# Kernel optimization log

Measured on AMD Instinct MI355X. Metric: run time of the kernel, lower is better.

Reference implementation:

```python
import jax, jax.numpy as jnp
import numpy as np

A = 4096          # agents
N_OBJ = 8192      # objects
IN_DIM = 16       # input_dim
EMBED = 128       # embedding_dim
MAX_OBJ = 16      # max set size
DEG = 8           # communicate in-degree (constant, target-major edges)
OBS_DEG = 8       # observe degree
POS_DIM = 2
ORIG = IN_DIM + POS_DIM   # 18, decoded element dim
THRES = 0.02              # duplicate filter distance threshold


def setup_inputs() -> dict:
    key = jax.random.key(0)
    ks = jax.random.split(key, 16)
    def lin(k, fi, fo):
        return (jax.random.normal(k, (fi, fo), jnp.float32) / np.float32(np.sqrt(fi)))
    obj_x = jax.random.normal(ks[0], (N_OBJ, IN_DIM), jnp.float32)
    obj_pos = jax.random.uniform(ks[1], (N_OBJ, POS_DIM), jnp.float32) * 10.0
    agent_pos = jax.random.uniform(ks[2], (A, POS_DIM), jnp.float32) * 10.0
    # (agent, observe, object) edges: row0 = agent, row1 = object (as in the torch HeteroData)
    obs_tgt = jnp.repeat(jnp.arange(A), OBS_DEG)
    obs_src = jax.random.randint(ks[3], (A * OBS_DEG,), 0, N_OBJ)
    obs_edge_index = jnp.stack([obs_tgt, obs_src])
    # (agent, communicate, agent) edges: row0 = source j, row1 = target i; target-major, constant degree
    tgt = jnp.repeat(jnp.arange(A), DEG)
    src = (tgt + 1 + jnp.tile(jnp.arange(DEG), A)) % A
    comm_edge_index = jnp.stack([src, tgt])
    return dict(
        obj_x=obj_x, obj_pos=obj_pos, agent_pos=agent_pos,
        enc_W1=lin(ks[4], ORIG, EMBED), enc_b1=jnp.zeros((EMBED,), jnp.float32),
        enc_W2=lin(ks[5], EMBED, EMBED), enc_b2=jnp.zeros((EMBED,), jnp.float32),
        mdec_Ws=lin(ks[6], EMBED, MAX_OBJ + 1), mdec_bs=jnp.zeros((MAX_OBJ + 1,), jnp.float32),
        mdec_Wx=lin(ks[7], EMBED, MAX_OBJ * ORIG), mdec_bx=jnp.zeros((MAX_OBJ * ORIG,), jnp.float32),
        menc_W1=lin(ks[8], ORIG, EMBED), menc_b1=jnp.zeros((EMBED,), jnp.float32),
        menc_W2=lin(ks[9], EMBED, EMBED), menc_b2=jnp.zeros((EMBED,), jnp.float32),
        dec_Ws=lin(ks[10], EMBED, MAX_OBJ + 1), dec_bs=jnp.zeros((MAX_OBJ + 1,), jnp.float32),
        dec_Wx=lin(ks[11], EMBED, MAX_OBJ * ORIG), dec_bx=jnp.zeros((MAX_OBJ * ORIG,), jnp.float32),
        obs_edge_index=obs_edge_index, comm_edge_index=comm_edge_index,
    )


def reference(obj_x, obj_pos, agent_pos,
              enc_W1, enc_b1, enc_W2, enc_b2,
              mdec_Ws, mdec_bs, mdec_Wx, mdec_bx,
              menc_W1, menc_b1, menc_W2, menc_b2,
              dec_Ws, dec_bs, dec_Wx, dec_bx,
              obs_edge_index, comm_edge_index):
    nA = agent_pos.shape[0]
    # ---- EncodeGNN: edge_index.flip -> source = object (row1), target = agent (row0)
    o = obs_edge_index[1]
    a = obs_edge_index[0]
    # message: [x_j, posx_j - posa_i] (position='rel')
    msg = jnp.concatenate([obj_x[o], obj_pos[o] - agent_pos[a]], axis=-1)      # [E_obs, ORIG]
    h = jax.nn.relu(msg @ enc_W1 + enc_b1)
    enc = jax.ops.segment_sum(h, a, num_segments=nA) @ enc_W2 + enc_b2         # [A, EMBED]
    # ---- MergeGNN message: decode source embedding per communicate edge
    j = comm_edge_index[0]
    i = comm_edge_index[1]
    zj = enc[j]                                                                 # [E, EMBED]
    npred = jnp.argmax(zj @ mdec_Ws + mdec_bs, axis=-1)                         # predicted set size per edge
    elems = (zj @ mdec_Wx + mdec_bx).reshape(-1, MAX_OBJ, ORIG)                 # [E, MAX_OBJ, ORIG]
    # update_rel_pos: decoded_pos += pos_j - pos_i
    relpos = (agent_pos[j] - agent_pos[i])[:, None, :]
    elems = jnp.concatenate([elems[..., :-POS_DIM], elems[..., -POS_DIM:] + relpos], axis=-1)
    valid = jnp.arange(MAX_OBJ)[None, :] < npred[:, None]                       # [E, MAX_OBJ]
    # ---- aggregate: edges are target-major with constant degree -> per-agent candidate pool
    deg = comm_edge_index.shape[1] // nA
    K = deg * MAX_OBJ
    cand = elems.reshape(nA, K, ORIG)
    v = valid.reshape(nA, K)
    # filter_duplicates (pos_only=True): pairwise distance on last POS_DIM dims
    pos = cand[..., -POS_DIM:]
    D = jnp.linalg.norm(pos[:, :, None, :] - pos[:, None, :, :], axis=-1)       # [A, K, K]
    tri = jnp.triu(jnp.ones((K, K), bool), k=1)
    dup = (D < THRES) & tri[None] & v[:, :, None] & v[:, None, :]
    keep = v & ~jnp.any(dup, axis=1)                                            # column is dup of an earlier row
    cnt = jnp.cumsum(keep.astype(jnp.int32), axis=1)
    keep = keep & (cnt <= MAX_OBJ - 1)                                          # cap at max_n - 1 kept elements
    # merge_encoder: masked set encode per agent
    hm = jax.nn.relu(cand @ menc_W1 + menc_b1) * keep[..., None]
    merged = hm.sum(axis=1) @ menc_W2 + menc_b2                                 # [A, EMBED]
    # ---- final decoder
    n2 = jnp.argmax(merged @ dec_Ws + dec_bs, axis=-1)
    decoded = (merged @ dec_Wx + dec_bx).reshape(nA, MAX_OBJ, ORIG)
    mask = jnp.arange(MAX_OBJ)[None, :] < n2[:, None]
    decoded = decoded * mask[..., None]                                         # padded+masked ragged set
    batch = jnp.broadcast_to(jnp.arange(nA)[:, None], (nA, MAX_OBJ))
    return decoded, batch, mask
```

## Files before the change

### kernel.cpp

```cpp
#include <hip/hip_runtime.h>

#define A_N   4096
#define EMBED 128
#define MAXO  16
#define DEG   8
#define OBSD  8
#define ORIG  18
#define KCAND 128
#define G     4
#define NBLK  (A_N / G)
#define NTHR  512
#define EL    (MAXO * ORIG)
#define NQ    (MAXO + 1)
#define THRES2 (0.02f * 0.02f)

__global__ __launch_bounds__(320) void prep_kernel(
    const float* __restrict__ enc_W2, const float* __restrict__ enc_b2,
    const float* __restrict__ mdec_Wx, const float* __restrict__ mdec_Ws,
    const float* __restrict__ mdec_bx, const float* __restrict__ mdec_bs,
    const float* __restrict__ menc_W2, const float* __restrict__ menc_b2,
    const float* __restrict__ dec_Wx, const float* __restrict__ dec_Ws,
    const float* __restrict__ dec_bx, const float* __restrict__ dec_bs,
    float* __restrict__ fWxA, float* __restrict__ fbxA,
    float* __restrict__ fWsA, float* __restrict__ fbsA,
    float* __restrict__ fWxB, float* __restrict__ fbxB,
    float* __restrict__ fWsB, float* __restrict__ fbsB)
{
    const int b = blockIdx.x, tid = threadIdx.x;
    const int side = b / 129, r = b % 129;
    const float* W2 = side ? menc_W2 : enc_W2;
    const float* b2 = side ? menc_b2 : enc_b2;
    const float* Wx = side ? dec_Wx : mdec_Wx;
    const float* Ws = side ? dec_Ws : mdec_Ws;
    const float* bx = side ? dec_bx : mdec_bx;
    const float* bs = side ? dec_bs : mdec_bs;
    float* oWx = side ? fWxB : fWxA;
    float* obx = side ? fbxB : fbxA;
    float* oWs = side ? fWsB : fWsA;
    float* obs_ = side ? fbsB : fbsA;

    __shared__ float rv[EMBED];
    if (tid < EMBED) rv[tid] = (r < EMBED) ? W2[r * EMBED + tid] : b2[tid];
    __syncthreads();

    if (tid < EL) {
        float acc = 0.f;
        for (int t = 0; t < EMBED; ++t) acc += rv[t] * Wx[t * EL + tid];
        if (r < EMBED) oWx[r * EL + tid] = acc;
        else           obx[tid] = acc + bx[tid];
    } else if (tid < EL + NQ) {
        const int q = tid - EL;
        float acc = 0.f;
        for (int t = 0; t < EMBED; ++t) acc += rv[t] * Ws[t * NQ + q];
        if (r < EMBED) oWs[r * NQ + q] = acc;
        else           obs_[q] = acc + bs[q];
    }
}

__global__ __launch_bounds__(NTHR, 8) void enc512_kernel(
    const float* __restrict__ obj_x, const float* __restrict__ obj_pos,
    const float* __restrict__ agent_pos,
    const float* __restrict__ enc_W1, const float* __restrict__ enc_b1,
    const float* __restrict__ fWxA, const float* __restrict__ fbxA,
    const float* __restrict__ fWsA, const float* __restrict__ fbsA,
    const int* __restrict__ obs_edge,
    float* __restrict__ elems_base, int* __restrict__ npred_out,
    float2* __restrict__ pxy_base)
{
    const int blk = blockIdx.x, tid = threadIdx.x;
    const int i0  = blk * G;
    const int col = tid & 127, q = tid >> 7;

    __shared__ int    on[G][OBSD];
    __shared__ float  msg[G * OBSD][20];
    __shared__ float4 SG[EMBED];
    __shared__ float  Lp[4][G * NQ];
    __shared__ float  lgts[G][NQ];
    __shared__ float4 Pp[2][EL];

    if (tid < G * OBSD) {
        const int g = tid >> 3, d = tid & 7;
        on[g][d] = obs_edge[A_N * OBSD + (i0 + g) * OBSD + d];
    }
    __syncthreads();
    for (int idx = tid; idx < G * OBSD * ORIG; idx += NTHR) {
        const int r = idx / ORIG, c = idx % ORIG;
        const int g = r >> 3, d = r & 7;
        const int o = on[g][d];
        float v;
        if (c < 16) v = obj_x[o * 16 + c];
        else        v = obj_pos[o * 2 + (c - 16)] - agent_pos[(i0 + g) * 2 + (c - 16)];
        msg[r][c] = v;
    }
    __syncthreads();

    {
        float w1[ORIG];
#pragma unroll
        for (int c = 0; c < ORIG; ++c) w1[c] = enc_W1[c * EMBED + col];
        const float b1 = enc_b1[col];
        float acc = 0.f;
#pragma unroll
        for (int d = 0; d < OBSD; ++d) {
            const int r = q * OBSD + d;
            const float4* mr = (const float4*)&msg[r][0];
            const float4 m0 = mr[0], m1 = mr[1], m2 = mr[2], m3 = mr[3];
            const float2 m4 = *(const float2*)&msg[r][16];
            float h = b1
                + m0.x*w1[0]  + m0.y*w1[1]  + m0.z*w1[2]  + m0.w*w1[3]
                + m1.x*w1[4]  + m1.y*w1[5]  + m1.z*w1[6]  + m1.w*w1[7]
                + m2.x*w1[8]  + m2.y*w1[9]  + m2.z*w1[10] + m2.w*w1[11]
                + m3.x*w1[12] + m3.y*w1[13] + m3.z*w1[14] + m3.w*w1[15]
                + m4.x*w1[16] + m4.y*w1[17];
            acc += fmaxf(h, 0.f);
        }
        ((float*)&SG[col])[q] = acc;
    }
    __syncthreads();

    {
        int u = tid;
        for (int pass = 0; pass < 2; ++pass) {
            if (u < 2 * EL) {
                const int h = (u >= EL) ? 1 : 0;
                const int e = u - h * EL;
                float4 acc = {0.f, 0.f, 0.f, 0.f};
                const int c0 = 64 * h;
#pragma unroll 8
                for (int c = c0; c < c0 + 64; ++c) {
                    const float4 s = SG[c];
                    const float  w = fWxA[c * EL + e];
                    acc.x += s.x * w; acc.y += s.y * w; acc.z += s.z * w; acc.w += s.w * w;
                }
                Pp[h][e] = acc;
            }
            u = NTHR + tid;
        }
    }
    __syncthreads();

    {
        const int p = tid >> 7, rem = tid & 127;
        if (rem < G * NQ) {
            const int g = rem / NQ, qq = rem % NQ;
            float v = 0.f;
            const int c0 = 32 * p;
#pragma unroll 8
            for (int c = c0; c < c0 + 32; ++c)
                v += ((const float*)&SG[c])[g] * fWsA[c * NQ + qq];
            Lp[p][rem] = v;
        }
    }
    __syncthreads();

    if (tid < EL) {
        const float4 a = Pp[0][tid], b = Pp[1][tid];
        const float bx = fbxA[tid];
        elems_base[(size_t)(i0 + 0) * EL + tid] = a.x + b.x + bx;
        elems_base[(size_t)(i0 + 1) * EL + tid] = a.y + b.y + bx;
        elems_base[(size_t)(i0 + 2) * EL + tid] = a.z + b.z + bx;
        elems_base[(size_t)(i0 + 3) * EL + tid] = a.w + b.w + bx;
    } else if (tid < EL + G * MAXO) {
        const int u = tid - EL;
        const int g = u >> 4, m = u & 15;
        const int e16 = m * ORIG + 16, e17 = e16 + 1;
        const float px = ((const float*)&Pp[0][e16])[g] + ((const float*)&Pp[1][e16])[g]
                       + fbxA[e16];
        const float py = ((const float*)&Pp[0][e17])[g] + ((const float*)&Pp[1][e17])[g]
                       + fbxA[e17];
        pxy_base[(size_t)(i0 + g) * MAXO + m] = make_float2(px, py);
    } else if (tid < EL + G * MAXO + G * NQ) {
        const int lq = tid - (EL + G * MAXO);
        const int g = lq / NQ, qq = lq % NQ;
        lgts[g][qq] = Lp[0][lq] + Lp[1][lq] + Lp[2][lq] + Lp[3][lq] + fbsA[qq];
    }
    __syncthreads();
    if (tid < G) {
        int best = 0; float bv = lgts[tid][0];
        for (int qq = 1; qq < NQ; ++qq) if (lgts[tid][qq] > bv) { bv = lgts[tid][qq]; best = qq; }
        npred_out[i0 + tid] = best;
    }
}

__global__ __launch_bounds__(NTHR, 8) void merge512_kernel(
    const float* __restrict__ agent_pos,
    const float* __restrict__ menc_W1, const float* __restrict__ menc_b1,
    const float* __restrict__ fWxB, const float* __restrict__ fbxB,
    const float* __restrict__ fWsB, const float* __restrict__ fbsB,
    const int* __restrict__ comm_edge,
    const float* __restrict__ elems_base, const int* __restrict__ npred,
    const float2* __restrict__ pxy_base,
    float* __restrict__ out_dec, float* __restrict__ out_batch,
    float* __restrict__ out_mask)
{
    const int blk = blockIdx.x, tid = threadIdx.x;
    const int i0  = blk * G;
    const int col = tid & 127, q = tid >> 7;
    const int lane = tid & 63, wv = tid >> 6;
    const int w = wv >> 1, half = wv & 1;

    __shared__ int    jn[G][DEG];
    __shared__ float  relx[G][DEG], rely[G][DEG];
    __shared__ int    npd[G][DEG];
    __shared__ float2 pxy[G][KCAND];
    __shared__ __align__(8)  int    vl[G][KCAND + 2];
    __shared__ __align__(16) float2 pv[G][KCAND];
    __shared__ int    wcv[G][2], kcv[G][2];
    __shared__ int    nv[G], kcnt[G];
    __shared__ int    klist[G][MAXO];
    __shared__ float  kc[G][MAXO][20];
    __shared__ float4 Hs[EMBED];
    __shared__ float  Lp[4][G * NQ];
    __shared__ float  lg2[G][NQ];
    __shared__ int    n2s[G];
    __shared__ float4 Pp[2][EL];

    if (tid < G * DEG) {
        const int g = tid >> 3, d = tid & 7;
        const int e = (i0 + g) * DEG + d;
        const int j  = comm_edge[e];
        const int ii = comm_edge[A_N * DEG + e];
        jn[g][d]  = j;
        relx[g][d] = agent_pos[j * 2 + 0] - agent_pos[ii * 2 + 0];
        rely[g][d] = agent_pos[j * 2 + 1] - agent_pos[ii * 2 + 1];
        npd[g][d] = npred[j];
    }
    __syncthreads();

    const int k = 64 * half + lane;
    const int kd = k >> 4, km = k & 15;
    float2 p;
    int val;
    {
        p = pxy_base[(size_t)jn[w][kd] * MAXO + km];
        p.x += relx[w][kd]; p.y += rely[w][kd];
        pxy[w][k] = p;
        val = (km < npd[w][kd]) ? 1 : 0;
        const unsigned long long bal = __ballot(val);
        const int pref = (int)__popcll(bal << (63 - lane));
        if (lane == 63) wcv[w][half] = (int)__popcll(bal);
        __syncthreads();
        const int base = half ? wcv[w][0] : 0;
        if (val) { vl[w][base + pref - 1] = k; pv[w][base + pref - 1] = p; }
        if (lane == 0 && half == 0) {
            const int tot = wcv[w][0] + wcv[w][1];
            nv[w] = tot;
            vl[w][tot] = 0x7fffffff;
            vl[w][tot + 1] = 0x7fffffff;
        }
        __syncthreads();
    }

    {
        const int nvg = nv[w];
        int dup = 0;
        for (int idx = 0; idx < nvg; idx += 2) {
            const int2   kk = *(const int2*)&vl[w][idx];
            const float4 pq = *(const float4*)&pv[w][idx];
            if (kk.x >= k) break;
            float dx = pq.x - p.x, dy = pq.y - p.y;
            dup |= (dx * dx + dy * dy < THRES2) ? 1 : 0;
            if (kk.y >= k) break;
            dx = pq.z - p.x; dy = pq.w - p.y;
            dup |= (dx * dx + dy * dy < THRES2) ? 1 : 0;
        }
        const int kp = (val && !dup) ? 1 : 0;
        const unsigned long long bal = __ballot(kp);
        const int pref = (int)__popcll(bal << (63 - lane));
        if (lane == 63) kcv[w][half] = (int)__popcll(bal);
        __syncthreads();
        const int cnt = (half ? kcv[w][0] : 0) + pref;
        if (kp && cnt <= MAXO - 1) klist[w][cnt - 1] = k;
        if (lane == 0 && half == 0) {
            const int tot = kcv[w][0] + kcv[w][1];
            kcnt[w] = (tot < MAXO - 1) ? tot : (MAXO - 1);
        }
        __syncthreads();
    }

    for (int idx = tid; idx < G * EL; idx += NTHR) {
        const int g = idx / EL, rem = idx % EL;
        const int s = rem / ORIG, c = rem % ORIG;
        if (s < kcnt[g]) {
            const int kk = klist[g][s], d = kk >> 4, m = kk & 15;
            float v;
            if (c < 16) v = elems_base[(size_t)jn[g][d] * EL + m * ORIG + c];
            else        v = (c == 16) ? pxy[g][kk].x : pxy[g][kk].y;
            kc[g][s][c] = v;
        }
    }
    __syncthreads();

    {
        float w1[ORIG];
#pragma unroll
        for (int c = 0; c < ORIG; ++c) w1[c] = menc_W1[c * EMBED + col];
        const float b1 = menc_b1[col];
        const int nk = kcnt[q];
        float hs = 0.f;
        for (int s = 0; s < nk; ++s) {
            const float4* mr = (const float4*)&kc[q][s][0];
            const float4 m0 = mr[0], m1 = mr[1], m2 = mr[2], m3 = mr[3];
            const float2 m4 = *(const float2*)&kc[q][s][16];
            float h = b1
                + m0.x*w1[0]  + m0.y*w1[1]  + m0.z*w1[2]  + m0.w*w1[3]
                + m1.x*w1[4]  + m1.y*w1[5]  + m1.z*w1[6]  + m1.w*w1[7]
                + m2.x*w1[8]  + m2.y*w1[9]  + m2.z*w1[10] + m2.w*w1[11]
                + m3.x*w1[12] + m3.y*w1[13] + m3.z*w1[14] + m3.w*w1[15]
                + m4.x*w1[16] + m4.y*w1[17];
            hs += fmaxf(h, 0.f);
        }
        ((float*)&Hs[col])[q] = hs;
    }
    __syncthreads();

    {
        int u = tid;
        for (int pass = 0; pass < 2; ++pass) {
            if (u < 2 * EL) {
                const int h = (u >= EL) ? 1 : 0;
                const int e = u - h * EL;
                float4 acc = {0.f, 0.f, 0.f, 0.f};
                const int c0 = 64 * h;
#pragma unroll 8
                for (int c = c0; c < c0 + 64; ++c) {
                    const float4 s = Hs[c];
                    const float  ww = fWxB[c * EL + e];
                    acc.x += s.x * ww; acc.y += s.y * ww; acc.z += s.z * ww; acc.w += s.w * ww;
                }
                Pp[h][e] = acc;
            }
            u = NTHR + tid;
        }
    }
    __syncthreads();

    {
        const int pth = tid >> 7, rem = tid & 127;
        if (rem < G * NQ) {
            const int g = rem / NQ, qq = rem % NQ;
            float v = 0.f;
            const int c0 = 32 * pth;
#pragma unroll 8
            for (int c = c0; c < c0 + 32; ++c)
                v += ((const float*)&Hs[c])[g] * fWsB[c * NQ + qq];
            Lp[pth][rem] = v;
        }
    }
    __syncthreads();

    float4 dreg = {0.f, 0.f, 0.f, 0.f};
    if (tid < EL) {
        const float4 a = Pp[0][tid], b = Pp[1][tid];
        const float bx = fbxB[tid];
        dreg.x = a.x + b.x + bx; dreg.y = a.y + b.y + bx;
        dreg.z = a.z + b.z + bx; dreg.w = a.w + b.w + bx;
    } else if (tid < EL + G * NQ) {
        const int lq = tid - EL;
        const int g = lq / NQ, qq = lq % NQ;
        lg2[g][qq] = Lp[0][lq] + Lp[1][lq] + Lp[2][lq] + Lp[3][lq] + fbsB[qq];
    }
    __syncthreads();
    if (tid < G) {
        int best = 0; float bv = lg2[tid][0];
        for (int qq = 1; qq < NQ; ++qq) if (lg2[tid][qq] > bv) { bv = lg2[tid][qq]; best = qq; }
        n2s[tid] = best;
    }
    __syncthreads();

    if (tid < EL) {
        const int m = tid / ORIG;
        out_dec[(size_t)(i0 + 0) * EL + tid] = (m < n2s[0]) ? dreg.x : 0.f;
        out_dec[(size_t)(i0 + 1) * EL + tid] = (m < n2s[1]) ? dreg.y : 0.f;
        out_dec[(size_t)(i0 + 2) * EL + tid] = (m < n2s[2]) ? dreg.z : 0.f;
        out_dec[(size_t)(i0 + 3) * EL + tid] = (m < n2s[3]) ? dreg.w : 0.f;
    } else if (tid >= NTHR - G * MAXO) {
        const int idx = tid - (NTHR - G * MAXO);
        const int g = idx >> 4, m = idx & 15;
        out_batch[(i0 + g) * MAXO + m] = (float)(i0 + g);
        out_mask[(i0 + g) * MAXO + m]  = (m < n2s[g]) ? 1.f : 0.f;
    }
}

extern "C" void kernel_launch(void* const* d_in, const int* in_sizes, int n_in,
                              void* d_out, int out_size, void* d_ws, size_t ws_size,
                              hipStream_t stream)
{
    const float* obj_x     = (const float*)d_in[0];
    const float* obj_pos   = (const float*)d_in[1];
    const float* agent_pos = (const float*)d_in[2];
    const float* enc_W1    = (const float*)d_in[3];
    const float* enc_b1    = (const float*)d_in[4];
    const float* enc_W2    = (const float*)d_in[5];
    const float* enc_b2    = (const float*)d_in[6];
    const float* mdec_Ws   = (const float*)d_in[7];
    const float* mdec_bs   = (const float*)d_in[8];
    const float* mdec_Wx   = (const float*)d_in[9];
    const float* mdec_bx   = (const float*)d_in[10];
    const float* menc_W1   = (const float*)d_in[11];
    const float* menc_b1   = (const float*)d_in[12];
    const float* menc_W2   = (const float*)d_in[13];
    const float* menc_b2   = (const float*)d_in[14];
    const float* dec_Ws    = (const float*)d_in[15];
    const float* dec_bs    = (const float*)d_in[16];
    const float* dec_Wx    = (const float*)d_in[17];
    const float* dec_bx    = (const float*)d_in[18];
    const int*   obs_edge  = (const int*)d_in[19];
    const int*   comm_edge = (const int*)d_in[20];

    char* ws = (char*)d_ws;
    size_t off = 0;
    float*  elems_base = (float*)(ws + off);  off += (size_t)A_N * EL * sizeof(float);
    int*    npred      = (int*)(ws + off);    off += (size_t)A_N * sizeof(int);
    float2* pxy_base   = (float2*)(ws + off); off += (size_t)A_N * MAXO * sizeof(float2);
    float*  fWxA = (float*)(ws + off);        off += (size_t)EMBED * EL * sizeof(float);
    float*  fbxA = (float*)(ws + off);        off += (size_t)EL * sizeof(float);
    float*  fWsA = (float*)(ws + off);        off += (size_t)EMBED * NQ * sizeof(float);
    float*  fbsA = (float*)(ws + off);        off += 32 * sizeof(float);
    float*  fWxB = (float*)(ws + off);        off += (size_t)EMBED * EL * sizeof(float);
    float*  fbxB = (float*)(ws + off);        off += (size_t)EL * sizeof(float);
    float*  fWsB = (float*)(ws + off);        off += (size_t)EMBED * NQ * sizeof(float);
    float*  fbsB = (float*)(ws + off);        off += 32 * sizeof(float);

    float* out_dec   = (float*)d_out;
    float* out_batch = out_dec + (size_t)A_N * EL;
    float* out_mask  = out_batch + (size_t)A_N * MAXO;

    prep_kernel<<<258, 320, 0, stream>>>(
        enc_W2, enc_b2, mdec_Wx, mdec_Ws, mdec_bx, mdec_bs,
        menc_W2, menc_b2, dec_Wx, dec_Ws, dec_bx, dec_bs,
        fWxA, fbxA, fWsA, fbsA, fWxB, fbxB, fWsB, fbsB);

    enc512_kernel<<<NBLK, NTHR, 0, stream>>>(
        obj_x, obj_pos, agent_pos, enc_W1, enc_b1,
        fWxA, fbxA, fWsA, fbsA, obs_edge,
        elems_base, npred, pxy_base);

    merge512_kernel<<<NBLK, NTHR, 0, stream>>>(
        agent_pos, menc_W1, menc_b1,
        fWxB, fbxB, fWsB, fbsB, comm_edge,
        elems_base, npred, pxy_base, out_dec, out_batch, out_mask);
}
```

Measured before the change: 152.5 us.

## Cut block barriers by fusing logit matvec into decoder pass and inlining edge loads

Both kernels drop the shared-memory staging of edge indices and neighbour data, so each thread reads comm/obs edges and agent positions directly from global memory, which removes a barrier. The second pass of the Wx matvec and the Ws logit matvec now run together in disjoint thread ranges under one barrier, with the logit partials split two ways instead of four. The argmax reads the partials directly and no longer goes through a separate reduction stage and barrier. This removes about three __syncthreads per kernel, at the cost of repeated global index loads and a more uneven thread workload.

```diff
diff --git a/kernel.cpp b/kernel.cpp
--- a/kernel.cpp
+++ b/kernel.cpp
@@ -71,22 +71,15 @@
     const int i0  = blk * G;
     const int col = tid & 127, q = tid >> 7;
 
-    __shared__ int    on[G][OBSD];
     __shared__ float  msg[G * OBSD][20];
     __shared__ float4 SG[EMBED];
-    __shared__ float  Lp[4][G * NQ];
-    __shared__ float  lgts[G][NQ];
+    __shared__ float  Lp[2][G * NQ];
     __shared__ float4 Pp[2][EL];
 
-    if (tid < G * OBSD) {
-        const int g = tid >> 3, d = tid & 7;
-        on[g][d] = obs_edge[A_N * OBSD + (i0 + g) * OBSD + d];
-    }
-    __syncthreads();
     for (int idx = tid; idx < G * OBSD * ORIG; idx += NTHR) {
         const int r = idx / ORIG, c = idx % ORIG;
         const int g = r >> 3, d = r & 7;
-        const int o = on[g][d];
+        const int o = obs_edge[A_N * OBSD + (i0 + g) * OBSD + d];
         float v;
         if (c < 16) v = obj_x[o * 16 + c];
         else        v = obj_pos[o * 2 + (c - 16)] - agent_pos[(i0 + g) * 2 + (c - 16)];
@@ -119,36 +112,39 @@
     __syncthreads();
 
     {
-        int u = tid;
-        for (int pass = 0; pass < 2; ++pass) {
-            if (u < 2 * EL) {
-                const int h = (u >= EL) ? 1 : 0;
-                const int e = u - h * EL;
-                float4 acc = {0.f, 0.f, 0.f, 0.f};
-                const int c0 = 64 * h;
-#pragma unroll 8
-                for (int c = c0; c < c0 + 64; ++c) {
-                    const float4 s = SG[c];
-                    const float  w = fWxA[c * EL + e];
-                    acc.x += s.x * w; acc.y += s.y * w; acc.z += s.z * w; acc.w += s.w * w;
-                }
-                Pp[h][e] = acc;
+        {
+            const int u = tid;
+            const int h = (u >= EL) ? 1 : 0;
+            const int e = u - h * EL;
+            float4 acc = {0.f, 0.f, 0.f, 0.f};
+            const int c0 = 64 * h;
+#pragma unroll 8
+            for (int c = c0; c < c0 + 64; ++c) {
+                const float4 s = SG[c];
+                const float  w = fWxA[c * EL + e];
+                acc.x += s.x * w; acc.y += s.y * w; acc.z += s.z * w; acc.w += s.w * w;
             }
-            u = NTHR + tid;
-        }
-    }
-    __syncthreads();
-
-    {
-        const int p = tid >> 7, rem = tid & 127;
-        if (rem < G * NQ) {
-            const int g = rem / NQ, qq = rem % NQ;
+            Pp[h][e] = acc;
+        }
+        if (tid < 64) {
+            const int e = (NTHR + tid) - EL;
+            float4 acc = {0.f, 0.f, 0.f, 0.f};
+#pragma unroll 8
+            for (int c = 64; c < 128; ++c) {
+                const float4 s = SG[c];
+                const float  w = fWxA[c * EL + e];
+                acc.x += s.x * w; acc.y += s.y * w; acc.z += s.z * w; acc.w += s.w * w;
+            }
+            Pp[1][e] = acc;
+        } else if (tid < 64 + 2 * G * NQ) {
+            const int lu = tid - 64, pp = lu / (G * NQ), lq = lu % (G * NQ);
+            const int g = lq / NQ, qq = lq % NQ;
             float v = 0.f;
-            const int c0 = 32 * p;
-#pragma unroll 8
-            for (int c = c0; c < c0 + 32; ++c)
+            const int c0 = 64 * pp;
+#pragma unroll 8
+            for (int c = c0; c < c0 + 64; ++c)
                 v += ((const float*)&SG[c])[g] * fWsA[c * NQ + qq];
-            Lp[p][rem] = v;
+            Lp[pp][lq] = v;
         }
     }
     __syncthreads();
@@ -169,16 +165,14 @@
         const float py = ((const float*)&Pp[0][e17])[g] + ((const float*)&Pp[1][e17])[g]
                        + fbxA[e17];
         pxy_base[(size_t)(i0 + g) * MAXO + m] = make_float2(px, py);
-    } else if (tid < EL + G * MAXO + G * NQ) {
-        const int lq = tid - (EL + G * MAXO);
-        const int g = lq / NQ, qq = lq % NQ;
-        lgts[g][qq] = Lp[0][lq] + Lp[1][lq] + Lp[2][lq] + Lp[3][lq] + fbsA[qq];
-    }
-    __syncthreads();
-    if (tid < G) {
-        int best = 0; float bv = lgts[tid][0];
-        for (int qq = 1; qq < NQ; ++qq) if (lgts[tid][qq] > bv) { bv = lgts[tid][qq]; best = qq; }
-        npred_out[i0 + tid] = best;
+    } else if (tid >= 448 && tid < 448 + G) {
+        const int g = tid - 448;
+        int best = 0; float bv = -3.0e38f;
+        for (int qq = 0; qq < NQ; ++qq) {
+            const float v = Lp[0][g * NQ + qq] + Lp[1][g * NQ + qq] + fbsA[qq];
+            if (v > bv) { bv = v; best = qq; }
+        }
+        npred_out[i0 + g] = best;
     }
 }
 
@@ -199,9 +193,6 @@
     const int lane = tid & 63, wv = tid >> 6;
     const int w = wv >> 1, half = wv & 1;
 
-    __shared__ int    jn[G][DEG];
-    __shared__ float  relx[G][DEG], rely[G][DEG];
-    __shared__ int    npd[G][DEG];
     __shared__ float2 pxy[G][KCAND];
     __shared__ __align__(8)  int    vl[G][KCAND + 2];
     __shared__ __align__(16) float2 pv[G][KCAND];
@@ -210,32 +201,21 @@
     __shared__ int    klist[G][MAXO];
     __shared__ float  kc[G][MAXO][20];
     __shared__ float4 Hs[EMBED];
-    __shared__ float  Lp[4][G * NQ];
-    __shared__ float  lg2[G][NQ];
+    __shared__ float  Lp[2][G * NQ];
     __shared__ int    n2s[G];
     __shared__ float4 Pp[2][EL];
 
-    if (tid < G * DEG) {
-        const int g = tid >> 3, d = tid & 7;
-        const int e = (i0 + g) * DEG + d;
-        const int j  = comm_edge[e];
-        const int ii = comm_edge[A_N * DEG + e];
-        jn[g][d]  = j;
-        relx[g][d] = agent_pos[j * 2 + 0] - agent_pos[ii * 2 + 0];
-        rely[g][d] = agent_pos[j * 2 + 1] - agent_pos[ii * 2 + 1];
-        npd[g][d] = npred[j];
-    }
-    __syncthreads();
-
     const int k = 64 * half + lane;
     const int kd = k >> 4, km = k & 15;
-    float2 p;
-    int val;
-    {
-        p = pxy_base[(size_t)jn[w][kd] * MAXO + km];
-        p.x += relx[w][kd]; p.y += rely[w][kd];
-        pxy[w][k] = p;
-        val = (km < npd[w][kd]) ? 1 : 0;
+    const int e_edge = (i0 + w) * DEG + kd;
+    const int jsrc = comm_edge[e_edge];
+    const int itgt = comm_edge[A_N * DEG + e_edge];
+    float2 p = pxy_base[(size_t)jsrc * MAXO + km];
+    p.x += agent_pos[jsrc * 2 + 0] - agent_pos[itgt * 2 + 0];
+    p.y += agent_pos[jsrc * 2 + 1] - agent_pos[itgt * 2 + 1];
+    const int val = (km < npred[jsrc]) ? 1 : 0;
+    pxy[w][k] = p;
+    {
         const unsigned long long bal = __ballot(val);
         const int pref = (int)__popcll(bal << (63 - lane));
         if (lane == 63) wcv[w][half] = (int)__popcll(bal);
@@ -283,8 +263,9 @@
         const int s = rem / ORIG, c = rem % ORIG;
         if (s < kcnt[g]) {
             const int kk = klist[g][s], d = kk >> 4, m = kk & 15;
+            const int j = comm_edge[(i0 + g) * DEG + d];
             float v;
-            if (c < 16) v = elems_base[(size_t)jn[g][d] * EL + m * ORIG + c];
+            if (c < 16) v = elems_base[(size_t)j * EL + m * ORIG + c];
             else        v = (c == 16) ? pxy[g][kk].x : pxy[g][kk].y;
             kc[g][s][c] = v;
         }
@@ -315,36 +296,39 @@
     __syncthreads();
 
     {
-        int u = tid;
-        for (int pass = 0; pass < 2; ++pass) {
-            if (u < 2 * EL) {
-                const int h = (u >= EL) ? 1 : 0;
-                const int e = u - h * EL;
-                float4 acc = {0.f, 0.f, 0.f, 0.f};
-                const int c0 = 64 * h;
-#pragma unroll 8
-                for (int c = c0; c < c0 + 64; ++c) {
-                    const float4 s = Hs[c];
-                    const float  ww = fWxB[c * EL + e];
-                    acc.x += s.x * ww; acc.y += s.y * ww; acc.z += s.z * ww; acc.w += s.w * ww;
-                }
-                Pp[h][e] = acc;
+        {
+            const int u = tid;
+            const int h = (u >= EL) ? 1 : 0;
+            const int e = u - h * EL;
+            float4 acc = {0.f, 0.f, 0.f, 0.f};
+            const int c0 = 64 * h;
+#pragma unroll 8
+            for (int c = c0; c < c0 + 64; ++c) {
+                const float4 s = Hs[c];
+                const float  ww = fWxB[c * EL + e];
+                acc.x += s.x * ww; acc.y += s.y * ww; acc.z += s.z * ww; acc.w += s.w * ww;
             }
-            u = NTHR + tid;
-        }
-    }
-    __syncthreads();
-
-    {
-        const int pth = tid >> 7, rem = tid & 127;
-        if (rem < G * NQ) {
-            const int g = rem / NQ, qq = rem % NQ;
+            Pp[h][e] = acc;
+        }
+        if (tid < 64) {
+            const int e = (NTHR + tid) - EL;
+            float4 acc = {0.f, 0.f, 0.f, 0.f};
+#pragma unroll 8
+            for (int c = 64; c < 128; ++c) {
+                const float4 s = Hs[c];
+                const float  ww = fWxB[c * EL + e];
+                acc.x += s.x * ww; acc.y += s.y * ww; acc.z += s.z * ww; acc.w += s.w * ww;
+            }
+            Pp[1][e] = acc;
+        } else if (tid < 64 + 2 * G * NQ) {
+            const int lu = tid - 64, pp = lu / (G * NQ), lq = lu % (G * NQ);
+            const int g = lq / NQ, qq = lq % NQ;
             float v = 0.f;
-            const int c0 = 32 * pth;
-#pragma unroll 8
-            for (int c = c0; c < c0 + 32; ++c)
+            const int c0 = 64 * pp;
+#pragma unroll 8
+            for (int c = c0; c < c0 + 64; ++c)
                 v += ((const float*)&Hs[c])[g] * fWsB[c * NQ + qq];
-            Lp[pth][rem] = v;
+            Lp[pp][lq] = v;
         }
     }
     __syncthreads();
@@ -355,16 +339,14 @@
         const float bx = fbxB[tid];
         dreg.x = a.x + b.x + bx; dreg.y = a.y + b.y + bx;
         dreg.z = a.z + b.z + bx; dreg.w = a.w + b.w + bx;
-    } else if (tid < EL + G * NQ) {
-        const int lq = tid - EL;
-        const int g = lq / NQ, qq = lq % NQ;
-        lg2[g][qq] = Lp[0][lq] + Lp[1][lq] + Lp[2][lq] + Lp[3][lq] + fbsB[qq];
-    }
-    __syncthreads();
-    if (tid < G) {
-        int best = 0; float bv = lg2[tid][0];
-        for (int qq = 1; qq < NQ; ++qq) if (lg2[tid][qq] > bv) { bv = lg2[tid][qq]; best = qq; }
-        n2s[tid] = best;
+    } else if (tid >= 448 && tid < 448 + G) {
+        const int g = tid - 448;
+        int best = 0; float bv = -3.0e38f;
+        for (int qq = 0; qq < NQ; ++qq) {
+            const float v = Lp[0][g * NQ + qq] + Lp[1][g * NQ + qq] + fbsB[qq];
+            if (v > bv) { bv = v; best = qq; }
+        }
+        n2s[g] = best;
     }
     __syncthreads();
 
```

Result: no change. 150.5 us (-1.3%).
